# Performance work log

Hardware: AMD Instinct MI355X
Metric: run time of the kernel (lower is better)

Reference implementation:

```python
import jax, jax.numpy as jnp
import numpy as np
import math

B, N, D, K = 4, 4096, 1024, 8


def setup_inputs() -> dict:
    key = jax.random.key(0)
    ks = jax.random.split(key, 9)
    s = 0.02
    return {
        "summaries": jax.random.normal(ks[0], (B, N, D), dtype=jnp.float32),
        "Wq": jax.random.normal(ks[1], (D, D), dtype=jnp.float32) * s,
        "bq": jnp.zeros((D,), dtype=jnp.float32),
        "Wk": jax.random.normal(ks[2], (D, D), dtype=jnp.float32) * s,
        "bk": jnp.zeros((D,), dtype=jnp.float32),
        "Wv": jax.random.normal(ks[3], (D, D), dtype=jnp.float32) * s,
        "bv": jnp.zeros((D,), dtype=jnp.float32),
        "Wo": jax.random.normal(ks[4], (D, D), dtype=jnp.float32) * s,
        "bo": jnp.zeros((D,), dtype=jnp.float32),
    }


def reference(summaries, Wq, bq, Wk, bk, Wv, bv, Wo, bo):
    b_, n_, d_ = summaries.shape
    q = summaries @ Wq + bq
    k = summaries @ Wk + bk
    v = summaries @ Wv + bv
    # [B, N, N] causal scores
    scores = jnp.einsum("bnd,bmd->bnm", q, k) / math.sqrt(d_)
    causal = jnp.triu(jnp.full((n_, n_), -jnp.inf, dtype=scores.dtype), k=1)
    scores = scores + causal
    # top-k sparse attention (N > K here, matching the torch branch)
    topk_vals, topk_idx = jax.lax.top_k(scores, K)  # [B, N, K]
    bi = jnp.arange(b_)[:, None, None]
    ri = jnp.arange(n_)[None, :, None]
    sparse = jnp.full_like(scores, -jnp.inf).at[bi, ri, topk_idx].set(topk_vals)
    attn = jax.nn.softmax(sparse, axis=-1)
    out = jnp.einsum("bnm,bmd->bnd", attn, v)
    return out @ Wo + bo
```

## Files before the change

### kernel.cpp

```cpp
#include <hip/hip_runtime.h>
#include <cstdint>
#include <cstddef>

#define B_ 4
#define N_ 4096
#define D_ 1024
#define CAND 16
#define M_ (B_*N_)
#define MD_ ((size_t)M_ * D_)
#define DD_ ((size_t)D_ * D_)

typedef __attribute__((ext_vector_type(8))) short short8;
typedef __attribute__((ext_vector_type(4))) float floatx4;

__device__ __align__(16) float          g_Qf[MD_];
__device__ __align__(16) float          g_Kf[MD_];
__device__ __align__(16) unsigned short g_Qb[MD_];
__device__ __align__(16) unsigned short g_Kb[MD_];
__device__ __align__(16) float          g_Vf[MD_];
__device__ __align__(16) unsigned short g_AO[MD_];
__device__ __align__(16) unsigned short g_X0[MD_];
__device__ __align__(16) unsigned short g_X1[MD_];
__device__ __align__(16) unsigned short g_Wq0T[DD_];
__device__ __align__(16) unsigned short g_Wq1T[DD_];
__device__ __align__(16) unsigned short g_Wk0T[DD_];
__device__ __align__(16) unsigned short g_Wk1T[DD_];
__device__ __align__(16) unsigned short g_WvT[DD_];
__device__ __align__(16) unsigned short g_WoT[DD_];
__device__ __align__(16) float          g_S[(size_t)B_ * N_ * N_];
__device__ __align__(16) int            g_cand[(size_t)M_ * CAND];
__device__ __align__(16) int            g_t8i[(size_t)M_ * 8];
__device__ __align__(16) float          g_t8w[(size_t)M_ * 8];

__device__ __forceinline__ float b2f(unsigned short u){
  return __uint_as_float(((unsigned int)u) << 16);
}
__device__ __forceinline__ unsigned short f2b(float f){
  unsigned int b = __float_as_uint(f);
  b += 0x7fffu + ((b >> 16) & 1u);
  return (unsigned short)(b >> 16);
}
__device__ __forceinline__ void split2(float x, unsigned short& h0,
                                       unsigned short& h1){
  h0 = f2b(x);
  float r1 = x - b2f(h0);
  h1 = f2b(r1);
}

__device__ __forceinline__ void gl_lds16(const void* g, void* l){
  __builtin_amdgcn_global_load_lds(
      (const __attribute__((address_space(1))) unsigned int*)g,
      (__attribute__((address_space(3))) unsigned int*)l, 16, 0, 0);
}

__global__ __launch_bounds__(256)
void transpose2(const float* __restrict__ Wv, const float* __restrict__ Wo){
  __shared__ float tile[32][33];
  const float* src = blockIdx.z ? Wo : Wv;
  unsigned short* dst = blockIdx.z ? g_WoT : g_WvT;
  int tx = threadIdx.x, ty = threadIdx.y;
  int n0 = blockIdx.x * 32, k0 = blockIdx.y * 32;
  for (int r = ty; r < 32; r += 8) tile[r][tx] = src[(size_t)(k0 + r) * D_ + n0 + tx];
  __syncthreads();
  for (int r = ty; r < 32; r += 8) dst[(size_t)(n0 + r) * D_ + k0 + tx] = f2b(tile[tx][r]);
}

__global__ __launch_bounds__(256)
void split_wT(const float* __restrict__ Wq, const float* __restrict__ Wk){
  __shared__ float tile[32][33];
  const float* src = blockIdx.z ? Wk : Wq;
  unsigned short* d0 = blockIdx.z ? g_Wk0T : g_Wq0T;
  unsigned short* d1 = blockIdx.z ? g_Wk1T : g_Wq1T;
  int tx = threadIdx.x, ty = threadIdx.y;
  int n0 = blockIdx.x * 32, k0 = blockIdx.y * 32;
  for (int r = ty; r < 32; r += 8) tile[r][tx] = src[(size_t)(k0 + r) * D_ + n0 + tx];
  __syncthreads();
  for (int r = ty; r < 32; r += 8){
    unsigned short h0, h1;
    split2(tile[tx][r], h0, h1);
    size_t o = (size_t)(n0 + r) * D_ + k0 + tx;
    d0[o] = h0; d1[o] = h1;
  }
}

__global__ __launch_bounds__(256)
void split_x(const float* __restrict__ X){
  size_t i = ((size_t)blockIdx.x * 256 + threadIdx.x) * 4;
  if (i >= MD_) return;
  float4 x = *(const float4*)&X[i];
  ushort4 u0, u1;
  split2(x.x, u0.x, u1.x);
  split2(x.y, u0.y, u1.y);
  split2(x.z, u0.z, u1.z);
  split2(x.w, u0.w, u1.w);
  *(ushort4*)&g_X0[i] = u0;
  *(ushort4*)&g_X1[i] = u1;
}

__global__ __launch_bounds__(256, 2)
void qk_split_gemm(const float* __restrict__ bq, const float* __restrict__ bk){
  int p = blockIdx.x;
  int lin = (p & 7) * 256 + (p >> 3);
  int mt = lin >> 4;
  int sub = lin & 15;
  int which = sub >> 3;
  int nt = sub & 7;

  const unsigned short* __restrict__ B0 = which ? g_Wk0T : g_Wq0T;
  const unsigned short* __restrict__ B1 = which ? g_Wk1T : g_Wq1T;
  const float* __restrict__ bias = which ? bk : bq;
  float* __restrict__ outf = which ? g_Kf : g_Qf;
  unsigned short* __restrict__ outb = which ? g_Kb : g_Qb;

  __shared__ unsigned short __align__(16) As0[128 * 64];
  __shared__ unsigned short __align__(16) As1[128 * 64];
  __shared__ unsigned short __align__(16) Bs0[128 * 64];
  __shared__ unsigned short __align__(16) Bs1[128 * 64];

  int tid = threadIdx.x;
  size_t m0 = (size_t)mt * 128;
  int n0 = nt * 128;
  int l = tid & 63, wid = tid >> 6;
  int wm = (wid >> 1) * 64, wn = (wid & 1) * 64;
  int quad = l >> 4, lr = l & 15;

  floatx4 acc[4][4];
  #pragma unroll
  for (int i = 0; i < 4; i++)
    #pragma unroll
    for (int j = 0; j < 4; j++) acc[i][j] = (floatx4)0.0f;

  for (int k0 = 0; k0 < D_; k0 += 64){
    #pragma unroll
    for (int c = 0; c < 4; c++){
      int d = c * 4096 + tid * 16;
      int rw = d >> 7;
      int sc = ((d & 127) ^ ((rw & 7) << 4)) >> 1;
      size_t ao = (m0 + rw) * D_ + k0 + sc;
      size_t bo = (size_t)(n0 + rw) * D_ + k0 + sc;
      gl_lds16(&g_X0[ao], &As0[d >> 1]);
      gl_lds16(&g_X1[ao], &As1[d >> 1]);
      gl_lds16(&B0[bo], &Bs0[d >> 1]);
      gl_lds16(&B1[bo], &Bs1[d >> 1]);
    }
    __syncthreads();
    #pragma unroll
    for (int kk = 0; kk < 2; kk++){
      short8 a0[4], a1[4], b0[4], b1[4];
      #pragma unroll
      for (int i = 0; i < 4; i++){
        int rw = wm + i * 16 + lr;
        int byt = rw * 128 + ((kk * 64 + quad * 16) ^ ((rw & 7) << 4));
        a0[i] = *(const short8*)&As0[byt >> 1];
        a1[i] = *(const short8*)&As1[byt >> 1];
      }
      #pragma unroll
      for (int j = 0; j < 4; j++){
        int rw = wn + j * 16 + lr;
        int byt = rw * 128 + ((kk * 64 + quad * 16) ^ ((rw & 7) << 4));
        b0[j] = *(const short8*)&Bs0[byt >> 1];
        b1[j] = *(const short8*)&Bs1[byt >> 1];
      }
      #pragma unroll
      for (int i = 0; i < 4; i++)
        #pragma unroll
        for (int j = 0; j < 4; j++){
          acc[i][j] = __builtin_amdgcn_mfma_f32_16x16x32_bf16(a0[i], b1[j], acc[i][j], 0, 0, 0);
          acc[i][j] = __builtin_amdgcn_mfma_f32_16x16x32_bf16(a1[i], b0[j], acc[i][j], 0, 0, 0);
          acc[i][j] = __builtin_amdgcn_mfma_f32_16x16x32_bf16(a0[i], b0[j], acc[i][j], 0, 0, 0);
        }
    }
    __syncthreads();
  }
  #pragma unroll
  for (int i = 0; i < 4; i++)
    #pragma unroll
    for (int j = 0; j < 4; j++)
      #pragma unroll
      for (int rg = 0; rg < 4; rg++){
        size_t row = m0 + wm + i * 16 + quad * 4 + rg;
        int col = n0 + wn + j * 16 + lr;
        float val = acc[i][j][rg] + bias[col];
        outf[row * D_ + col] = val;
        outb[row * D_ + col] = f2b(val);
      }
}

__global__ __launch_bounds__(256)
void gemm_bf16(const float* __restrict__ bias, float* __restrict__ Cout, int sel){
  const unsigned short* Asrc = sel ? g_AO : g_X0;
  const unsigned short* Bt = sel ? g_WoT : g_WvT;
  float* C = sel ? Cout : g_Vf;
  __shared__ unsigned short __align__(16) As[128 * 32];
  __shared__ unsigned short __align__(16) Bs[128 * 32];
  int p = blockIdx.x;
  int lin = (p & 7) * 128 + (p >> 3);
  int mt = lin >> 3;
  int nt = lin & 7;
  int tid = threadIdx.x;
  size_t m0 = (size_t)mt * 128;
  int n0 = nt * 128;
  int l = tid & 63, wid = tid >> 6;
  int wm = (wid >> 1) * 64, wn = (wid & 1) * 64;
  int quad = l >> 4, lr = l & 15;
  int srow = tid >> 2, scol = (tid & 3) * 8;
  floatx4 acc[4][4];
  #pragma unroll
  for (int i = 0; i < 4; i++)
    #pragma unroll
    for (int j = 0; j < 4; j++) acc[i][j] = (floatx4)0.0f;

  for (int k0 = 0; k0 < D_; k0 += 32){
    #pragma unroll
    for (int it = 0; it < 2; it++){
      int r = srow + it * 64;
      int so = r * 32 + scol;
      gl_lds16(&Asrc[(m0 + r) * D_ + k0 + scol], &As[so]);
      gl_lds16(&Bt[(size_t)(n0 + r) * D_ + k0 + scol], &Bs[so]);
    }
    __syncthreads();
    short8 af[4], bf[4];
    #pragma unroll
    for (int i = 0; i < 4; i++) af[i] = *(short8*)&As[(wm + i * 16 + lr) * 32 + quad * 8];
    #pragma unroll
    for (int j = 0; j < 4; j++) bf[j] = *(short8*)&Bs[(wn + j * 16 + lr) * 32 + quad * 8];
    #pragma unroll
    for (int i = 0; i < 4; i++)
      #pragma unroll
      for (int j = 0; j < 4; j++)
        acc[i][j] = __builtin_amdgcn_mfma_f32_16x16x32_bf16(af[i], bf[j], acc[i][j], 0, 0, 0);
    __syncthreads();
  }
  #pragma unroll
  for (int i = 0; i < 4; i++)
    #pragma unroll
    for (int j = 0; j < 4; j++)
      #pragma unroll
      for (int rg = 0; rg < 4; rg++){
        size_t row = m0 + wm + i * 16 + quad * 4 + rg;
        int col = n0 + wn + j * 16 + lr;
        C[row * D_ + col] = acc[i][j][rg] + bias[col];
      }
}

__global__ __launch_bounds__(256)
void scores_gemm(){
  int jt = blockIdx.x, it = blockIdx.y, b = blockIdx.z;
  if (jt > it) return;
  __shared__ unsigned short __align__(16) As[128 * 32];
  __shared__ unsigned short __align__(16) Bs[128 * 32];
  int tid = threadIdx.x;
  size_t am0 = (size_t)b * N_ + it * 128;
  size_t bn0 = (size_t)b * N_ + jt * 128;
  int l = tid & 63, wid = tid >> 6;
  int wm = (wid >> 1) * 64, wn = (wid & 1) * 64;
  int quad = l >> 4, lr = l & 15;
  int srow = tid >> 2, scol = (tid & 3) * 8;
  floatx4 acc[4][4];
  #pragma unroll
  for (int i = 0; i < 4; i++)
    #pragma unroll
    for (int j = 0; j < 4; j++) acc[i][j] = (floatx4)0.0f;

  for (int k0 = 0; k0 < D_; k0 += 32){
    #pragma unroll
    for (int it2 = 0; it2 < 2; it2++){
      int r = srow + it2 * 64;
      int so = r * 32 + scol;
      gl_lds16(&g_Qb[(am0 + r) * D_ + k0 + scol], &As[so]);
      gl_lds16(&g_Kb[(bn0 + r) * D_ + k0 + scol], &Bs[so]);
    }
    __syncthreads();
    short8 af[4], bf[4];
    #pragma unroll
    for (int i = 0; i < 4; i++) af[i] = *(short8*)&As[(wm + i * 16 + lr) * 32 + quad * 8];
    #pragma unroll
    for (int j = 0; j < 4; j++) bf[j] = *(short8*)&Bs[(wn + j * 16 + lr) * 32 + quad * 8];
    #pragma unroll
    for (int i = 0; i < 4; i++)
      #pragma unroll
      for (int j = 0; j < 4; j++)
        acc[i][j] = __builtin_amdgcn_mfma_f32_16x16x32_bf16(af[i], bf[j], acc[i][j], 0, 0, 0);
    __syncthreads();
  }
  #pragma unroll
  for (int i = 0; i < 4; i++)
    #pragma unroll
    for (int j = 0; j < 4; j++)
      #pragma unroll
      for (int rg = 0; rg < 4; rg++){
        int row = it * 128 + wm + i * 16 + quad * 4 + rg;
        int col = jt * 128 + wn + j * 16 + lr;
        float v = acc[i][j][rg] * 0.03125f;
        if (col > row) v = -3.0e38f;
        g_S[((size_t)b * N_ + row) * N_ + col] = v;
      }
}

__global__ __launch_bounds__(256)
void row_topk(){
  __shared__ float lv[CAND * 256];
  __shared__ int   li[CAND * 256];
  int w = threadIdx.x >> 6, l = threadIdx.x & 63;
  int g = threadIdx.x;
  int i = blockIdx.x * 4 + w;
  int irow = i & (N_ - 1);
  const float* Srow = &g_S[(size_t)i * N_];
  #pragma unroll
  for (int u = 0; u < CAND; u++){ lv[u * 256 + g] = -3.0e38f; li[u * 256 + g] = -1; }
  float vmin = -3.0e38f; int pmin = 0;
  for (int j0 = l * 4; j0 <= irow; j0 += 256){
    float4 v4 = *(const float4*)&Srow[j0];
    #pragma unroll
    for (int e = 0; e < 4; e++){
      float v = (&v4.x)[e];
      if (v > vmin){
        lv[pmin * 256 + g] = v; li[pmin * 256 + g] = j0 + e;
        float m = lv[g]; int p = 0;
        #pragma unroll
        for (int u = 1; u < CAND; u++){ float x = lv[u * 256 + g]; if (x < m){ m = x; p = u; } }
        vmin = m; pmin = p;
      }
    }
  }
  float mv = lv[g]; int mp = 0;
  #pragma unroll
  for (int u = 1; u < CAND; u++){ float x = lv[u * 256 + g]; if (x > mv){ mv = x; mp = u; } }
  int mj = li[mp * 256 + g];
  for (int rd = 0; rd < CAND; rd++){
    float bv = mv; int bj = mj; int bl = l;
    #pragma unroll
    for (int off = 32; off >= 1; off >>= 1){
      float ov = __shfl_xor(bv, off);
      int oj = __shfl_xor(bj, off);
      int ol = __shfl_xor(bl, off);
      if (ov > bv || (ov == bv && ol < bl)){ bv = ov; bj = oj; bl = ol; }
    }
    bool valid = (bv > -2.9e38f);
    if (l == 0) g_cand[(size_t)i * CAND + rd] = valid ? bj : -1;
    if (valid && bl == l){
      lv[mp * 256 + g] = -3.0e38f;
      mv = lv[g]; mp = 0;
      #pragma unroll
      for (int u = 1; u < CAND; u++){ float x = lv[u * 256 + g]; if (x > mv){ mv = x; mp = u; } }
      mj = li[mp * 256 + g];
    }
  }
}

__global__ __launch_bounds__(256)
void rescore_top8(){
  int i = blockIdx.x;
  int b = i >> 12;
  int tid = threadIdx.x, l = tid & 63, w = tid >> 6;
  __shared__ double cs[CAND];
  __shared__ int cid[CAND];
  if (tid < CAND) cid[tid] = g_cand[(size_t)i * CAND + tid];
  __syncthreads();
  double q[16];
  #pragma unroll
  for (int u = 0; u < 16; u++) q[u] = (double)g_Qf[(size_t)i * D_ + l + 64 * u];
  for (int c = w * 4; c < w * 4 + 4; c++){
    int j = cid[c];
    double s = 0.0;
    if (j >= 0){
      size_t ko = ((size_t)(b * N_ + j)) * D_;
      #pragma unroll
      for (int u = 0; u < 16; u++) s = fma(q[u], (double)g_Kf[ko + l + 64 * u], s);
    }
    #pragma unroll
    for (int off = 32; off >= 1; off >>= 1) s += __shfl_down(s, off);
    if (l == 0) cs[c] = (j >= 0) ? s * 0.03125 : -1.0e300;
  }
  __syncthreads();
  if (tid == 0){
    double v8[8]; int i8[8];
    bool used[CAND];
    for (int u = 0; u < CAND; u++) used[u] = false;
    for (int rk = 0; rk < 8; rk++){
      double best = -1.0e300; int bp = -1;
      for (int c = 0; c < CAND; c++)
        if (!used[c] && cid[c] >= 0 && cs[c] > best){ best = cs[c]; bp = c; }
      if (bp >= 0){ used[bp] = true; v8[rk] = best; i8[rk] = cid[bp]; }
      else { v8[rk] = -1.0e300; i8[rk] = -1; }
    }
    if (i8[0] < 0){ i8[0] = i & (N_ - 1); v8[0] = 0.0; }
    double mx = v8[0];
    double e[8]; double Z = 0.0;
    for (int rk = 0; rk < 8; rk++){
      e[rk] = (i8[rk] >= 0) ? exp(v8[rk] - mx) : 0.0;
      Z += e[rk];
    }
    for (int rk = 0; rk < 8; rk++){
      g_t8i[(size_t)i * 8 + rk] = i8[rk];
      g_t8w[(size_t)i * 8 + rk] = (float)(e[rk] / Z);
    }
  }
}

__global__ __launch_bounds__(256)
void gather_v(){
  int i = blockIdx.x;
  int b = i >> 12;
  int tid = threadIdx.x;
  __shared__ float ws8[8];
  __shared__ int id8[8];
  if (tid < 8){ ws8[tid] = g_t8w[(size_t)i * 8 + tid]; id8[tid] = g_t8i[(size_t)i * 8 + tid]; }
  __syncthreads();
  int d0 = tid * 4;
  float a0 = 0.f, a1 = 0.f, a2 = 0.f, a3 = 0.f;
  #pragma unroll
  for (int rk = 0; rk < 8; rk++){
    int j = id8[rk];
    if (j < 0) continue;
    float wgt = ws8[rk];
    float4 vv = *(const float4*)&g_Vf[((size_t)(b * N_ + j)) * D_ + d0];
    a0 += wgt * vv.x; a1 += wgt * vv.y; a2 += wgt * vv.z; a3 += wgt * vv.w;
  }
  ushort4 o;
  o.x = f2b(a0); o.y = f2b(a1); o.z = f2b(a2); o.w = f2b(a3);
  *(ushort4*)&g_AO[(size_t)i * D_ + d0] = o;
}

extern "C" void kernel_launch(void* const* d_in, const int* in_sizes, int n_in,
                              void* d_out, int out_size, void* d_ws, size_t ws_size,
                              hipStream_t stream){
  const float* S  = (const float*)d_in[0];
  const float* Wq = (const float*)d_in[1];
  const float* bq = (const float*)d_in[2];
  const float* Wk = (const float*)d_in[3];
  const float* bk = (const float*)d_in[4];
  const float* Wv = (const float*)d_in[5];
  const float* bv = (const float*)d_in[6];
  const float* Wo = (const float*)d_in[7];
  const float* bo = (const float*)d_in[8];
  float* out = (float*)d_out;
  (void)d_ws; (void)ws_size; (void)in_sizes; (void)n_in; (void)out_size;

  transpose2<<<dim3(32, 32, 2), dim3(32, 8), 0, stream>>>(Wv, Wo);
  split_wT<<<dim3(32, 32, 2), dim3(32, 8), 0, stream>>>(Wq, Wk);
  split_x<<<dim3(M_), 256, 0, stream>>>(S);
  qk_split_gemm<<<dim3(2048), 256, 0, stream>>>(bq, bk);
  gemm_bf16<<<dim3(1024), 256, 0, stream>>>(bv, nullptr, 0);
  scores_gemm<<<dim3(32, 32, 4), 256, 0, stream>>>();
  row_topk<<<dim3(M_ / 4), 256, 0, stream>>>();
  rescore_top8<<<dim3(M_), 256, 0, stream>>>();
  gather_v<<<dim3(M_), 256, 0, stream>>>();
  gemm_bf16<<<dim3(1024), 256, 0, stream>>>(bo, out, 1);
}
```

Baseline: 1.057 ms.

## Widen GEMM K-tile to 128 with XOR-swizzled LDS layout in bf16 and scores kernels

The bf16 projection GEMM and the causal scores GEMM now stage a 128-wide K slice per iteration instead of 32. Each block does four MFMA sub-steps per stage, so there are a quarter as many barriers and load rounds. The LDS layout uses an XOR swizzle on the 16-byte column chunk, keyed by row, to avoid bank conflicts on the 256-byte row stride. LDS per block grows to 64 KB, and the launch bounds now request 2 blocks per CU, which may limit occupancy and latency hiding because the loads are still not double-buffered.

```diff
diff --git a/kernel.cpp b/kernel.cpp
--- a/kernel.cpp
+++ b/kernel.cpp
@@ -186,13 +186,13 @@
       }
 }
 
-__global__ __launch_bounds__(256)
+__global__ __launch_bounds__(256, 2)
 void gemm_bf16(const float* __restrict__ bias, float* __restrict__ Cout, int sel){
   const unsigned short* Asrc = sel ? g_AO : g_X0;
   const unsigned short* Bt = sel ? g_WoT : g_WvT;
   float* C = sel ? Cout : g_Vf;
-  __shared__ unsigned short __align__(16) As[128 * 32];
-  __shared__ unsigned short __align__(16) Bs[128 * 32];
+  __shared__ unsigned short __align__(16) As[128 * 128];
+  __shared__ unsigned short __align__(16) Bs[128 * 128];
   int p = blockIdx.x;
   int lin = (p & 7) * 128 + (p >> 3);
   int mt = lin >> 3;
@@ -203,32 +203,43 @@
   int l = tid & 63, wid = tid >> 6;
   int wm = (wid >> 1) * 64, wn = (wid & 1) * 64;
   int quad = l >> 4, lr = l & 15;
-  int srow = tid >> 2, scol = (tid & 3) * 8;
   floatx4 acc[4][4];
   #pragma unroll
   for (int i = 0; i < 4; i++)
     #pragma unroll
     for (int j = 0; j < 4; j++) acc[i][j] = (floatx4)0.0f;
 
-  for (int k0 = 0; k0 < D_; k0 += 32){
-    #pragma unroll
-    for (int it = 0; it < 2; it++){
-      int r = srow + it * 64;
-      int so = r * 32 + scol;
-      gl_lds16(&Asrc[(m0 + r) * D_ + k0 + scol], &As[so]);
-      gl_lds16(&Bt[(size_t)(n0 + r) * D_ + k0 + scol], &Bs[so]);
-    }
-    __syncthreads();
-    short8 af[4], bf[4];
-    #pragma unroll
-    for (int i = 0; i < 4; i++) af[i] = *(short8*)&As[(wm + i * 16 + lr) * 32 + quad * 8];
-    #pragma unroll
-    for (int j = 0; j < 4; j++) bf[j] = *(short8*)&Bs[(wn + j * 16 + lr) * 32 + quad * 8];
-    #pragma unroll
-    for (int i = 0; i < 4; i++)
-      #pragma unroll
-      for (int j = 0; j < 4; j++)
-        acc[i][j] = __builtin_amdgcn_mfma_f32_16x16x32_bf16(af[i], bf[j], acc[i][j], 0, 0, 0);
+  for (int k0 = 0; k0 < D_; k0 += 128){
+    #pragma unroll
+    for (int c = 0; c < 8; c++){
+      int d = c * 4096 + tid * 16;
+      int rw = d >> 8;
+      int sc = ((d & 255) ^ ((rw & 7) << 4)) >> 1;
+      gl_lds16(&Asrc[(m0 + rw) * D_ + k0 + sc], &As[d >> 1]);
+      gl_lds16(&Bt[(size_t)(n0 + rw) * D_ + k0 + sc], &Bs[d >> 1]);
+    }
+    __syncthreads();
+    #pragma unroll
+    for (int kk = 0; kk < 4; kk++){
+      short8 af[4], bf[4];
+      #pragma unroll
+      for (int i = 0; i < 4; i++){
+        int rw = wm + i * 16 + lr;
+        int byt = rw * 256 + ((kk * 64 + quad * 16) ^ ((rw & 7) << 4));
+        af[i] = *(const short8*)&As[byt >> 1];
+      }
+      #pragma unroll
+      for (int j = 0; j < 4; j++){
+        int rw = wn + j * 16 + lr;
+        int byt = rw * 256 + ((kk * 64 + quad * 16) ^ ((rw & 7) << 4));
+        bf[j] = *(const short8*)&Bs[byt >> 1];
+      }
+      #pragma unroll
+      for (int i = 0; i < 4; i++)
+        #pragma unroll
+        for (int j = 0; j < 4; j++)
+          acc[i][j] = __builtin_amdgcn_mfma_f32_16x16x32_bf16(af[i], bf[j], acc[i][j], 0, 0, 0);
+    }
     __syncthreads();
   }
   #pragma unroll
@@ -243,44 +254,55 @@
       }
 }
 
-__global__ __launch_bounds__(256)
+__global__ __launch_bounds__(256, 2)
 void scores_gemm(){
   int jt = blockIdx.x, it = blockIdx.y, b = blockIdx.z;
   if (jt > it) return;
-  __shared__ unsigned short __align__(16) As[128 * 32];
-  __shared__ unsigned short __align__(16) Bs[128 * 32];
+  __shared__ unsigned short __align__(16) As[128 * 128];
+  __shared__ unsigned short __align__(16) Bs[128 * 128];
   int tid = threadIdx.x;
   size_t am0 = (size_t)b * N_ + it * 128;
   size_t bn0 = (size_t)b * N_ + jt * 128;
   int l = tid & 63, wid = tid >> 6;
   int wm = (wid >> 1) * 64, wn = (wid & 1) * 64;
   int quad = l >> 4, lr = l & 15;
-  int srow = tid >> 2, scol = (tid & 3) * 8;
   floatx4 acc[4][4];
   #pragma unroll
   for (int i = 0; i < 4; i++)
     #pragma unroll
     for (int j = 0; j < 4; j++) acc[i][j] = (floatx4)0.0f;
 
-  for (int k0 = 0; k0 < D_; k0 += 32){
-    #pragma unroll
-    for (int it2 = 0; it2 < 2; it2++){
-      int r = srow + it2 * 64;
-      int so = r * 32 + scol;
-      gl_lds16(&g_Qb[(am0 + r) * D_ + k0 + scol], &As[so]);
-      gl_lds16(&g_Kb[(bn0 + r) * D_ + k0 + scol], &Bs[so]);
-    }
-    __syncthreads();
-    short8 af[4], bf[4];
-    #pragma unroll
-    for (int i = 0; i < 4; i++) af[i] = *(short8*)&As[(wm + i * 16 + lr) * 32 + quad * 8];
-    #pragma unroll
-    for (int j = 0; j < 4; j++) bf[j] = *(short8*)&Bs[(wn + j * 16 + lr) * 32 + quad * 8];
-    #pragma unroll
-    for (int i = 0; i < 4; i++)
-      #pragma unroll
-      for (int j = 0; j < 4; j++)
-        acc[i][j] = __builtin_amdgcn_mfma_f32_16x16x32_bf16(af[i], bf[j], acc[i][j], 0, 0, 0);
+  for (int k0 = 0; k0 < D_; k0 += 128){
+    #pragma unroll
+    for (int c = 0; c < 8; c++){
+      int d = c * 4096 + tid * 16;
+      int rw = d >> 8;
+      int sc = ((d & 255) ^ ((rw & 7) << 4)) >> 1;
+      gl_lds16(&g_Qb[(am0 + rw) * D_ + k0 + sc], &As[d >> 1]);
+      gl_lds16(&g_Kb[(bn0 + rw) * D_ + k0 + sc], &Bs[d >> 1]);
+    }
+    __syncthreads();
+    #pragma unroll
+    for (int kk = 0; kk < 4; kk++){
+      short8 af[4], bf[4];
+      #pragma unroll
+      for (int i = 0; i < 4; i++){
+        int rw = wm + i * 16 + lr;
+        int byt = rw * 256 + ((kk * 64 + quad * 16) ^ ((rw & 7) << 4));
+        af[i] = *(const short8*)&As[byt >> 1];
+      }
+      #pragma unroll
+      for (int j = 0; j < 4; j++){
+        int rw = wn + j * 16 + lr;
+        int byt = rw * 256 + ((kk * 64 + quad * 16) ^ ((rw & 7) << 4));
+        bf[j] = *(const short8*)&Bs[byt >> 1];
+      }
+      #pragma unroll
+      for (int i = 0; i < 4; i++)
+        #pragma unroll
+        for (int j = 0; j < 4; j++)
+          acc[i][j] = __builtin_amdgcn_mfma_f32_16x16x32_bf16(af[i], bf[j], acc[i][j], 0, 0, 0);
+    }
     __syncthreads();
   }
   #pragma unroll
```

New measurement: 998.6 us. 1.06x faster.
